# Performance work log

Hardware: AMD Instinct MI355X
Metric: run time of the kernel (lower is better)

Reference implementation:

```python
import jax, jax.numpy as jnp
import numpy as np

B = 8
FEAT = 256
HID = 256
NCLS = 80
SIZES = [(128, 128), (64, 64), (32, 32), (16, 16), (8, 8)]
DELTA_XY = 0.1   # dd_delta_range_xy
DELTA_WH = 2.0   # dd_delta_range_wh
PRIOR_P = 0.01   # prior_cls_prob


def _priors():
    # prior_cxcy: normalized grid centers per pyramid level (sine_pos_encodings id maps,
    # normalize=True with all-ones masks). prior_wh: (1/fW, 1/fH) per level.
    cxcy, wh = [], []
    for (h, w) in SIZES:
        cy = (jnp.arange(h, dtype=jnp.float32) + 0.5) / h
        cx = (jnp.arange(w, dtype=jnp.float32) + 0.5) / w
        gx, gy = jnp.meshgrid(cx, cy, indexing='xy')           # [h, w]
        cxcy.append(jnp.stack([gx, gy], axis=-1).reshape(h * w, 2))
        wh.append(jnp.broadcast_to(jnp.array([1.0 / w, 1.0 / h], jnp.float32), (h * w, 2)))
    return jnp.concatenate(cxcy, axis=0), jnp.concatenate(wh, axis=0)  # [N,2], [N,2]


def _mlp(x, Wh, bh, Wo, bo):
    # Linear(feat->hidden) + ReLU, then Linear(hidden->out)
    h = jax.nn.relu(jnp.einsum('bnf,hf->bnh', x, Wh) + bh)
    return jnp.einsum('bnh,oh->bno', h, Wo) + bo


def setup_inputs() -> dict:
    key = jax.random.key(0)
    ks = jax.random.split(key, 12)
    inp = {}
    for i, (h, w) in enumerate(SIZES):
        inp[f'fm{i}'] = jax.random.normal(ks[i], (B, FEAT, h, w), dtype=jnp.float32)
    s_in = 1.0 / np.sqrt(FEAT)
    s_h = 1.0 / np.sqrt(HID)
    bias_value = float(-np.log((1.0 - PRIOR_P) / PRIOR_P))
    inp['cls_Wh'] = jax.random.normal(ks[5], (HID, FEAT), dtype=jnp.float32) * s_in
    inp['cls_bh'] = jnp.zeros((HID,), jnp.float32)
    inp['cls_Wo'] = jax.random.normal(ks[6], (NCLS, HID), dtype=jnp.float32) * s_h
    inp['cls_bo'] = jnp.full((NCLS,), bias_value, jnp.float32)  # focal prior bias init
    inp['box_Wh'] = jax.random.normal(ks[7], (HID, FEAT), dtype=jnp.float32) * s_in
    inp['box_bh'] = jnp.zeros((HID,), jnp.float32)
    inp['box_Wo'] = jax.random.normal(ks[8], (4, HID), dtype=jnp.float32) * s_h
    inp['box_bo'] = jnp.zeros((4,), jnp.float32)  # zero-init box bias
    return inp


def reference(fm0, fm1, fm2, fm3, fm4,
              cls_Wh, cls_bh, cls_Wo, cls_bo,
              box_Wh, box_bh, box_Wo, box_bo):
    fms = [fm0, fm1, fm2, fm3, fm4]
    # obj_feats: concat of flatten(2).permute(0,2,1) -> [B, N, FEAT]
    obj_feats = jnp.concatenate(
        [f.reshape(B, FEAT, -1).transpose(0, 2, 1) for f in fms], axis=1)
    cls_logits = _mlp(obj_feats, cls_Wh, cls_bh, cls_Wo, cls_bo)   # [B, N, NCLS]
    box_logits = _mlp(obj_feats, box_Wh, box_bh, box_Wo, box_bo)   # [B, N, 4]
    box_deltas = jnp.tanh(box_logits)
    prior_cxcy, prior_wh = _priors()
    pred_cxcy = prior_cxcy[None] + DELTA_XY * box_deltas[:, :, :2]
    pred_wh = prior_wh[None] * (DELTA_WH ** box_deltas[:, :, 2:])
    # pack [cls_logits | pred_boxes(cxcywh)] -> [B, N, NCLS+4]
    return jnp.concatenate([cls_logits, pred_cxcy, pred_wh], axis=-1)
```

## Files before the change

kernel.cpp:

```cpp
#include <hip/hip_runtime.h>
#include <math.h>
#include <stdint.h>

#define NTOK 21824

typedef __attribute__((ext_vector_type(8)))  short bf16x8;
typedef __attribute__((ext_vector_type(4)))  float f32x4;
typedef __attribute__((ext_vector_type(16))) float f32x16;

__device__ __forceinline__ uint32_t f2bf(float f) {
    uint32_t u = __builtin_bit_cast(uint32_t, f);
    return (u + 0x7FFFu + ((u >> 16) & 1u)) >> 16;
}
__device__ __forceinline__ uint32_t pkbf(float lo, float hi) {
    return f2bf(lo) | (f2bf(hi) << 16);
}

#define WOFF_CWH 0
#define WOFF_BWH 65536
#define WOFF_CWO 131072
#define WOFF_BWO 151552

__global__ void prep_weights(const float* __restrict__ cWh, const float* __restrict__ cWo,
                             const float* __restrict__ bWh, const float* __restrict__ bWo,
                             uint16_t* __restrict__ ws) {
    int i = blockIdx.x * 256 + threadIdx.x;
    if (i >= 155648) return;
    uint32_t v;
    if (i < 65536)       v = f2bf(cWh[i]);
    else if (i < 131072) v = f2bf(bWh[i - 65536]);
    else if (i < 151552) v = f2bf(cWo[i - 131072]);
    else { int j = i - 151552; v = (j < 1024) ? f2bf(bWo[j]) : 0u; }
    ws[i] = (uint16_t)v;
}

__global__ __launch_bounds__(512, 4) void dfd_fused(
    const float* __restrict__ fm0, const float* __restrict__ fm1,
    const float* __restrict__ fm2, const float* __restrict__ fm3,
    const float* __restrict__ fm4,
    const float* __restrict__ cls_bh, const float* __restrict__ cls_bo,
    const float* __restrict__ box_bh, const float* __restrict__ box_bo,
    const uint16_t* __restrict__ wbf,
    float* __restrict__ out)
{
    __shared__ uint16_t LB[64 * 512];
    uint16_t* Xs = LB;
    uint16_t* Hs = LB;

    const int tid  = threadIdx.x;
    const int lane = tid & 63;
    const int w    = tid >> 6;
    const int r    = lane & 15;
    const int q    = lane >> 4;
    const int n0   = blockIdx.x * 64;
    const int b    = blockIdx.y;

    const float* fm; int off, ls;
    if      (n0 < 16384) { fm = fm0; off = 0;     ls = 7; }
    else if (n0 < 20480) { fm = fm1; off = 16384; ls = 6; }
    else if (n0 < 21504) { fm = fm2; off = 20480; ls = 5; }
    else if (n0 < 21760) { fm = fm3; off = 21504; ls = 4; }
    else                 { fm = fm4; off = 21760; ls = 3; }
    const int dim = 1 << ls;
    const int hw  = dim * dim;
    const int p0  = n0 - off;

    {
        const int t  = lane;
        const int sw = (t & 7) << 3;
        const float* src = fm + (size_t)b * 256 * hw + p0 + t;
        #pragma unroll
        for (int i = 0; i < 8; ++i) {
            const int f = w * 4 + i * 32;
            const float x0 = src[(size_t)(f + 0) * hw];
            const float x1 = src[(size_t)(f + 1) * hw];
            const float x2 = src[(size_t)(f + 2) * hw];
            const float x3 = src[(size_t)(f + 3) * hw];
            uint2 pk; pk.x = pkbf(x0, x1); pk.y = pkbf(x2, x3);
            *reinterpret_cast<uint2*>(&Xs[t * 256 + (f ^ sw)]) = pk;
        }
    }
    __syncthreads();

    f32x16 acc[2][2];
    {
        #pragma unroll
        for (int mt = 0; mt < 2; ++mt)
            #pragma unroll
            for (int h = 0; h < 2; ++h)
                #pragma unroll
                for (int e = 0; e < 16; ++e) acc[mt][h][e] = 0.f;

        const int col = lane & 31;
        const int kh  = (lane >> 5) * 8;
        const uint16_t* Wc = wbf + WOFF_CWH + (w * 32 + col) * 256 + kh;
        const uint16_t* Wb = wbf + WOFF_BWH + (w * 32 + col) * 256 + kh;

        #pragma unroll
        for (int ks = 0; ks < 16; ++ks) {
            const bf16x8 bc = *(const bf16x8*)(Wc + ks * 16);
            const bf16x8 bb = *(const bf16x8*)(Wb + ks * 16);
            #pragma unroll
            for (int mt = 0; mt < 2; ++mt) {
                const int t = mt * 32 + col;
                const int k = (ks * 16 + kh) ^ ((t & 7) << 3);
                const bf16x8 a = *(const bf16x8*)&Xs[t * 256 + k];
                acc[mt][0] = __builtin_amdgcn_mfma_f32_32x32x16_bf16(a, bc, acc[mt][0], 0, 0, 0);
                acc[mt][1] = __builtin_amdgcn_mfma_f32_32x32x16_bf16(a, bb, acc[mt][1], 0, 0, 0);
            }
        }
    }
    __syncthreads();

    {
        const int col  = lane & 31;
        const float bc = cls_bh[w * 32 + col];
        const float bbx = box_bh[w * 32 + col];
        #pragma unroll
        for (int mt = 0; mt < 2; ++mt) {
            #pragma unroll
            for (int reg = 0; reg < 16; ++reg) {
                const int t  = mt * 32 + (reg & 3) + 8 * (reg >> 2) + 4 * (lane >> 5);
                const int sw = (t & 7) << 3;
                const int hh = w * 32 + col;
                Hs[t * 512 + ((hh)       ^ sw)] = (uint16_t)f2bf(fmaxf(acc[mt][0][reg] + bc, 0.f));
                Hs[t * 512 + ((256 + hh) ^ sw)] = (uint16_t)f2bf(fmaxf(acc[mt][1][reg] + bbx, 0.f));
            }
        }
    }
    __syncthreads();

    if (w < 5) {
        f32x4 c[4];
        #pragma unroll
        for (int m = 0; m < 4; ++m) c[m] = {0.f, 0.f, 0.f, 0.f};
        const uint16_t* Bw = wbf + WOFF_CWO + (w * 16 + r) * 256 + q * 8;
        #pragma unroll
        for (int kq = 0; kq < 8; ++kq) {
            const bf16x8 bfr = *(const bf16x8*)(Bw + kq * 32);
            #pragma unroll
            for (int m = 0; m < 4; ++m) {
                const int t = m * 16 + r;
                const int kcol = (kq * 32 + q * 8) ^ ((t & 7) << 3);
                const bf16x8 a = *(const bf16x8*)&Hs[t * 512 + kcol];
                c[m] = __builtin_amdgcn_mfma_f32_16x16x32_bf16(a, bfr, c[m], 0, 0, 0);
            }
        }
        const float bo_l = cls_bo[w * 16 + r];
        #pragma unroll
        for (int m = 0; m < 4; ++m)
            #pragma unroll
            for (int jj = 0; jj < 4; ++jj)
                out[((size_t)b * NTOK + n0 + m * 16 + q * 4 + jj) * 84 + w * 16 + r]
                    = c[m][jj] + bo_l;
    } else if (w < 7) {
        const int m0 = (w - 5) * 2;
        f32x4 c[2];
        c[0] = {0.f, 0.f, 0.f, 0.f}; c[1] = {0.f, 0.f, 0.f, 0.f};
        const uint16_t* Bw = wbf + WOFF_BWO + r * 256 + q * 8;
        #pragma unroll
        for (int kq = 0; kq < 8; ++kq) {
            const bf16x8 bfr = *(const bf16x8*)(Bw + kq * 32);
            #pragma unroll
            for (int mm = 0; mm < 2; ++mm) {
                const int t = (m0 + mm) * 16 + r;
                const int kcol = 256 + ((kq * 32 + q * 8) ^ ((t & 7) << 3));
                const bf16x8 a = *(const bf16x8*)&Hs[t * 512 + kcol];
                c[mm] = __builtin_amdgcn_mfma_f32_16x16x32_bf16(a, bfr, c[mm], 0, 0, 0);
            }
        }
        if (r < 4) {
            const float bo_l = box_bo[r];
            const float inv  = 1.0f / (float)dim;
            #pragma unroll
            for (int mm = 0; mm < 2; ++mm)
                #pragma unroll
                for (int jj = 0; jj < 4; ++jj) {
                    const int t = (m0 + mm) * 16 + q * 4 + jj;
                    const int p = p0 + t;
                    const float d = tanhf(c[mm][jj] + bo_l);
                    float val;
                    if (r == 0)      val = ((float)(p & (dim - 1)) + 0.5f) * inv + 0.1f * d;
                    else if (r == 1) val = ((float)(p >> ls) + 0.5f) * inv + 0.1f * d;
                    else             val = exp2f(d) * inv;
                    out[((size_t)b * NTOK + n0 + t) * 84 + 80 + r] = val;
                }
        }
    }
}

extern "C" void kernel_launch(void* const* d_in, const int* in_sizes, int n_in,
                              void* d_out, int out_size, void* d_ws, size_t ws_size,
                              hipStream_t stream) {
    uint16_t* ws = (uint16_t*)d_ws;
    prep_weights<<<608, 256, 0, stream>>>(
        (const float*)d_in[5],  (const float*)d_in[7],
        (const float*)d_in[9],  (const float*)d_in[11], ws);
    dim3 grid(NTOK / 64, 8);
    dfd_fused<<<grid, 512, 0, stream>>>(
        (const float*)d_in[0], (const float*)d_in[1], (const float*)d_in[2],
        (const float*)d_in[3], (const float*)d_in[4],
        (const float*)d_in[6],  (const float*)d_in[8],
        (const float*)d_in[10], (const float*)d_in[12],
        ws, (float*)d_out);
}
```

Measured before the change: 136.3 us.

## Swap MFMA operand roles so outputs are row-contiguous and vectorize stores

Transposes both GEMM stages so weights are the A operand and tokens the B operand. Each lane then holds consecutive hidden units or classes for one token, which allows packed bf16x4 hidden writes to LDS and float4 global stores of the output rows. The second-stage work is rebalanced across all 8 waves, where before waves 7 were idle and waves 5-6 did the box head. It also switches to the HIP bf16 intrinsic for packing. The risk is extra weight-fragment loads per wave and divergent branches on mh.

```diff
diff --git a/kernel.cpp b/kernel.cpp
--- a/kernel.cpp
+++ b/kernel.cpp
@@ -1,4 +1,5 @@
 #include <hip/hip_runtime.h>
+#include <hip/hip_bf16.h>
 #include <math.h>
 #include <stdint.h>
 
@@ -12,8 +13,10 @@
     uint32_t u = __builtin_bit_cast(uint32_t, f);
     return (u + 0x7FFFu + ((u >> 16) & 1u)) >> 16;
 }
-__device__ __forceinline__ uint32_t pkbf(float lo, float hi) {
-    return f2bf(lo) | (f2bf(hi) << 16);
+__device__ __forceinline__ uint32_t pkbf2(float lo, float hi) {
+    __hip_bfloat162 h = __float22bfloat162_rn(float2{lo, hi});
+    uint32_t r; __builtin_memcpy(&r, &h, 4);
+    return r;
 }
 
 #define WOFF_CWH 0
@@ -52,6 +55,8 @@
     const int w    = tid >> 6;
     const int r    = lane & 15;
     const int q    = lane >> 4;
+    const int col  = lane & 31;
+    const int hi   = lane >> 5;
     const int n0   = blockIdx.x * 64;
     const int b    = blockIdx.y;
 
@@ -76,7 +81,7 @@
             const float x1 = src[(size_t)(f + 1) * hw];
             const float x2 = src[(size_t)(f + 2) * hw];
             const float x3 = src[(size_t)(f + 3) * hw];
-            uint2 pk; pk.x = pkbf(x0, x1); pk.y = pkbf(x2, x3);
+            uint2 pk; pk.x = pkbf2(x0, x1); pk.y = pkbf2(x2, x3);
             *reinterpret_cast<uint2*>(&Xs[t * 256 + (f ^ sw)]) = pk;
         }
     }
@@ -87,104 +92,114 @@
         #pragma unroll
         for (int mt = 0; mt < 2; ++mt)
             #pragma unroll
-            for (int h = 0; h < 2; ++h)
+            for (int nt = 0; nt < 2; ++nt)
                 #pragma unroll
-                for (int e = 0; e < 16; ++e) acc[mt][h][e] = 0.f;
-
-        const int col = lane & 31;
-        const int kh  = (lane >> 5) * 8;
-        const uint16_t* Wc = wbf + WOFF_CWH + (w * 32 + col) * 256 + kh;
-        const uint16_t* Wb = wbf + WOFF_BWH + (w * 32 + col) * 256 + kh;
+                for (int e = 0; e < 16; ++e) acc[mt][nt][e] = 0.f;
+
+        const int hh0 = w * 64;
+        const uint16_t* Wbase = (w < 4) ? wbf + WOFF_CWH + hh0 * 256
+                                        : wbf + WOFF_BWH + (hh0 - 256) * 256;
+        const int kh = hi * 8;
+        const uint16_t* Wr = Wbase + col * 256 + kh;
+        const int sw0 = (col & 7) << 3;
 
         #pragma unroll
         for (int ks = 0; ks < 16; ++ks) {
-            const bf16x8 bc = *(const bf16x8*)(Wc + ks * 16);
-            const bf16x8 bb = *(const bf16x8*)(Wb + ks * 16);
-            #pragma unroll
-            for (int mt = 0; mt < 2; ++mt) {
-                const int t = mt * 32 + col;
-                const int k = (ks * 16 + kh) ^ ((t & 7) << 3);
-                const bf16x8 a = *(const bf16x8*)&Xs[t * 256 + k];
-                acc[mt][0] = __builtin_amdgcn_mfma_f32_32x32x16_bf16(a, bc, acc[mt][0], 0, 0, 0);
-                acc[mt][1] = __builtin_amdgcn_mfma_f32_32x32x16_bf16(a, bb, acc[mt][1], 0, 0, 0);
-            }
+            const bf16x8 a0 = *(const bf16x8*)(Wr + ks * 16);
+            const bf16x8 a1 = *(const bf16x8*)(Wr + 8192 + ks * 16);
+            const int kx = (ks * 16 + kh) ^ sw0;
+            const bf16x8 x0 = *(const bf16x8*)&Xs[col * 256 + kx];
+            const bf16x8 x1 = *(const bf16x8*)&Xs[(32 + col) * 256 + kx];
+            acc[0][0] = __builtin_amdgcn_mfma_f32_32x32x16_bf16(a0, x0, acc[0][0], 0, 0, 0);
+            acc[0][1] = __builtin_amdgcn_mfma_f32_32x32x16_bf16(a0, x1, acc[0][1], 0, 0, 0);
+            acc[1][0] = __builtin_amdgcn_mfma_f32_32x32x16_bf16(a1, x0, acc[1][0], 0, 0, 0);
+            acc[1][1] = __builtin_amdgcn_mfma_f32_32x32x16_bf16(a1, x1, acc[1][1], 0, 0, 0);
         }
     }
     __syncthreads();
 
     {
-        const int col  = lane & 31;
-        const float bc = cls_bh[w * 32 + col];
-        const float bbx = box_bh[w * 32 + col];
+        const int hh0 = w * 64;
+        const float* bh_ = (w < 4) ? cls_bh + hh0 : box_bh + (hh0 - 256);
         #pragma unroll
         for (int mt = 0; mt < 2; ++mt) {
             #pragma unroll
-            for (int reg = 0; reg < 16; ++reg) {
-                const int t  = mt * 32 + (reg & 3) + 8 * (reg >> 2) + 4 * (lane >> 5);
-                const int sw = (t & 7) << 3;
-                const int hh = w * 32 + col;
-                Hs[t * 512 + ((hh)       ^ sw)] = (uint16_t)f2bf(fmaxf(acc[mt][0][reg] + bc, 0.f));
-                Hs[t * 512 + ((256 + hh) ^ sw)] = (uint16_t)f2bf(fmaxf(acc[mt][1][reg] + bbx, 0.f));
+            for (int nt = 0; nt < 2; ++nt) {
+                const int t   = nt * 32 + col;
+                const int swt = (t & 7) << 3;
+                #pragma unroll
+                for (int g = 0; g < 4; ++g) {
+                    const int hb = mt * 32 + 8 * g + 4 * hi;
+                    const f32x4 bv = *(const f32x4*)(bh_ + hb);
+                    const float v0 = fmaxf(acc[mt][nt][4 * g + 0] + bv[0], 0.f);
+                    const float v1 = fmaxf(acc[mt][nt][4 * g + 1] + bv[1], 0.f);
+                    const float v2 = fmaxf(acc[mt][nt][4 * g + 2] + bv[2], 0.f);
+                    const float v3 = fmaxf(acc[mt][nt][4 * g + 3] + bv[3], 0.f);
+                    uint2 pk; pk.x = pkbf2(v0, v1); pk.y = pkbf2(v2, v3);
+                    *reinterpret_cast<uint2*>(&Hs[t * 512 + ((hh0 + hb) ^ swt)]) = pk;
+                }
             }
         }
     }
     __syncthreads();
 
-    if (w < 5) {
-        f32x4 c[4];
-        #pragma unroll
-        for (int m = 0; m < 4; ++m) c[m] = {0.f, 0.f, 0.f, 0.f};
-        const uint16_t* Bw = wbf + WOFF_CWO + (w * 16 + r) * 256 + q * 8;
+    {
+        const int nt2 = w & 3;
+        const int mh  = w >> 2;
+        const int t   = nt2 * 16 + r;
+        const int swt = (t & 7) << 3;
+        const uint16_t* hrow = &Hs[t * 512];
+
+        f32x4 c[3];
+        c[0] = {0.f,0.f,0.f,0.f}; c[1] = {0.f,0.f,0.f,0.f}; c[2] = {0.f,0.f,0.f,0.f};
+        const int m0 = mh * 3;
+        const uint16_t* WoA = wbf + WOFF_CWO + r * 256 + q * 8;
+        const uint16_t* WoB = wbf + WOFF_BWO + r * 256 + q * 8;
+
         #pragma unroll
         for (int kq = 0; kq < 8; ++kq) {
-            const bf16x8 bfr = *(const bf16x8*)(Bw + kq * 32);
-            #pragma unroll
-            for (int m = 0; m < 4; ++m) {
-                const int t = m * 16 + r;
-                const int kcol = (kq * 32 + q * 8) ^ ((t & 7) << 3);
-                const bf16x8 a = *(const bf16x8*)&Hs[t * 512 + kcol];
-                c[m] = __builtin_amdgcn_mfma_f32_16x16x32_bf16(a, bfr, c[m], 0, 0, 0);
+            const bf16x8 hb = *(const bf16x8*)&hrow[(kq * 32 + q * 8) ^ swt];
+            const bf16x8 aA = *(const bf16x8*)(WoA + (m0 + 0) * 4096 + kq * 32);
+            const bf16x8 aB = *(const bf16x8*)(WoA + (m0 + 1) * 4096 + kq * 32);
+            c[0] = __builtin_amdgcn_mfma_f32_16x16x32_bf16(aA, hb, c[0], 0, 0, 0);
+            c[1] = __builtin_amdgcn_mfma_f32_16x16x32_bf16(aB, hb, c[1], 0, 0, 0);
+            if (mh == 0) {
+                const bf16x8 aC = *(const bf16x8*)(WoA + 2 * 4096 + kq * 32);
+                c[2] = __builtin_amdgcn_mfma_f32_16x16x32_bf16(aC, hb, c[2], 0, 0, 0);
+            } else {
+                const bf16x8 hbb = *(const bf16x8*)&hrow[(256 + kq * 32 + q * 8) ^ swt];
+                const bf16x8 aC  = *(const bf16x8*)(WoB + kq * 32);
+                c[2] = __builtin_amdgcn_mfma_f32_16x16x32_bf16(aC, hbb, c[2], 0, 0, 0);
             }
         }
-        const float bo_l = cls_bo[w * 16 + r];
-        #pragma unroll
-        for (int m = 0; m < 4; ++m)
-            #pragma unroll
-            for (int jj = 0; jj < 4; ++jj)
-                out[((size_t)b * NTOK + n0 + m * 16 + q * 4 + jj) * 84 + w * 16 + r]
-                    = c[m][jj] + bo_l;
-    } else if (w < 7) {
-        const int m0 = (w - 5) * 2;
-        f32x4 c[2];
-        c[0] = {0.f, 0.f, 0.f, 0.f}; c[1] = {0.f, 0.f, 0.f, 0.f};
-        const uint16_t* Bw = wbf + WOFF_BWO + r * 256 + q * 8;
-        #pragma unroll
-        for (int kq = 0; kq < 8; ++kq) {
-            const bf16x8 bfr = *(const bf16x8*)(Bw + kq * 32);
-            #pragma unroll
-            for (int mm = 0; mm < 2; ++mm) {
-                const int t = (m0 + mm) * 16 + r;
-                const int kcol = 256 + ((kq * 32 + q * 8) ^ ((t & 7) << 3));
-                const bf16x8 a = *(const bf16x8*)&Hs[t * 512 + kcol];
-                c[mm] = __builtin_amdgcn_mfma_f32_16x16x32_bf16(a, bfr, c[mm], 0, 0, 0);
+
+        float* orow = out + ((size_t)b * NTOK + n0 + t) * 84;
+        const int ncls = (mh == 0) ? 3 : 2;
+        #pragma unroll
+        for (int i = 0; i < 3; ++i) {
+            if (i < ncls) {
+                const int m = m0 + i;
+                const f32x4 bo = *(const f32x4*)(cls_bo + m * 16 + q * 4);
+                f32x4 v;
+                #pragma unroll
+                for (int jj = 0; jj < 4; ++jj) v[jj] = c[i][jj] + bo[jj];
+                *(f32x4*)(orow + m * 16 + q * 4) = v;
             }
         }
-        if (r < 4) {
-            const float bo_l = box_bo[r];
-            const float inv  = 1.0f / (float)dim;
-            #pragma unroll
-            for (int mm = 0; mm < 2; ++mm)
-                #pragma unroll
-                for (int jj = 0; jj < 4; ++jj) {
-                    const int t = (m0 + mm) * 16 + q * 4 + jj;
-                    const int p = p0 + t;
-                    const float d = tanhf(c[mm][jj] + bo_l);
-                    float val;
-                    if (r == 0)      val = ((float)(p & (dim - 1)) + 0.5f) * inv + 0.1f * d;
-                    else if (r == 1) val = ((float)(p >> ls) + 0.5f) * inv + 0.1f * d;
-                    else             val = exp2f(d) * inv;
-                    out[((size_t)b * NTOK + n0 + t) * 84 + 80 + r] = val;
-                }
+        if (mh == 1 && q == 0) {
+            const f32x4 bo = *(const f32x4*)box_bo;
+            const float inv = 1.0f / (float)dim;
+            const int p = p0 + t;
+            const float d0 = tanhf(c[2][0] + bo[0]);
+            const float d1 = tanhf(c[2][1] + bo[1]);
+            const float d2 = tanhf(c[2][2] + bo[2]);
+            const float d3 = tanhf(c[2][3] + bo[3]);
+            f32x4 v;
+            v[0] = ((float)(p & (dim - 1)) + 0.5f) * inv + 0.1f * d0;
+            v[1] = ((float)(p >> ls) + 0.5f) * inv + 0.1f * d1;
+            v[2] = exp2f(d2) * inv;
+            v[3] = exp2f(d3) * inv;
+            *(f32x4*)(orow + 80) = v;
         }
     }
 }
```

After: 182.0 us. 1.34x slower.

## Make blocks persistent over four token tiles and prefetch next tile's features into registers

Applied to the files above, without the earlier changes.

Each block now handles four consecutive 64-token tiles instead of one, shrinking the grid to 86x8. The next tile's fp32 feature loads are issued into registers before the current tile's MFMA work, so global latency overlaps compute. The bf16 packing of inputs also switches to the hip_bf16 paired conversion intrinsic. The cost is 32 extra live registers per thread and fewer blocks (688) to spread over the CUs, which may hurt occupancy and load balance.

```diff
diff --git a/kernel.cpp b/kernel.cpp
--- a/kernel.cpp
+++ b/kernel.cpp
@@ -1,8 +1,12 @@
 #include <hip/hip_runtime.h>
+#include <hip/hip_bf16.h>
 #include <math.h>
 #include <stdint.h>
 
 #define NTOK 21824
+#define NTILES 341
+#define NITER 4
+#define GRIDX 86
 
 typedef __attribute__((ext_vector_type(8)))  short bf16x8;
 typedef __attribute__((ext_vector_type(4)))  float f32x4;
@@ -12,8 +16,10 @@
     uint32_t u = __builtin_bit_cast(uint32_t, f);
     return (u + 0x7FFFu + ((u >> 16) & 1u)) >> 16;
 }
-__device__ __forceinline__ uint32_t pkbf(float lo, float hi) {
-    return f2bf(lo) | (f2bf(hi) << 16);
+__device__ __forceinline__ uint32_t pkbf2(float lo, float hi) {
+    __hip_bfloat162 h = __float22bfloat162_rn(float2{lo, hi});
+    uint32_t r; __builtin_memcpy(&r, &h, 4);
+    return r;
 }
 
 #define WOFF_CWH 0
@@ -52,140 +58,171 @@
     const int w    = tid >> 6;
     const int r    = lane & 15;
     const int q    = lane >> 4;
-    const int n0   = blockIdx.x * 64;
+    const int col  = lane & 31;
+    const int hi   = lane >> 5;
     const int b    = blockIdx.y;
 
-    const float* fm; int off, ls;
-    if      (n0 < 16384) { fm = fm0; off = 0;     ls = 7; }
-    else if (n0 < 20480) { fm = fm1; off = 16384; ls = 6; }
-    else if (n0 < 21504) { fm = fm2; off = 20480; ls = 5; }
-    else if (n0 < 21760) { fm = fm3; off = 21504; ls = 4; }
-    else                 { fm = fm4; off = 21760; ls = 3; }
-    const int dim = 1 << ls;
-    const int hw  = dim * dim;
-    const int p0  = n0 - off;
-
-    {
-        const int t  = lane;
-        const int sw = (t & 7) << 3;
-        const float* src = fm + (size_t)b * 256 * hw + p0 + t;
+    auto lookup = [&](int n0, const float*& fm, int& off, int& ls) {
+        if      (n0 < 16384) { fm = fm0; off = 0;     ls = 7; }
+        else if (n0 < 20480) { fm = fm1; off = 16384; ls = 6; }
+        else if (n0 < 21504) { fm = fm2; off = 20480; ls = 5; }
+        else if (n0 < 21760) { fm = fm3; off = 21504; ls = 4; }
+        else                 { fm = fm4; off = 21760; ls = 3; }
+    };
+
+    float xr[32];
+    auto load_x = [&](int tl) {
+        const float* fmp; int offp, lsp;
+        const int nn = tl * 64;
+        lookup(nn, fmp, offp, lsp);
+        const int hwp = 1 << (2 * lsp);
+        const float* src = fmp + (size_t)b * 256 * hwp + (nn - offp) + lane;
         #pragma unroll
         for (int i = 0; i < 8; ++i) {
             const int f = w * 4 + i * 32;
-            const float x0 = src[(size_t)(f + 0) * hw];
-            const float x1 = src[(size_t)(f + 1) * hw];
-            const float x2 = src[(size_t)(f + 2) * hw];
-            const float x3 = src[(size_t)(f + 3) * hw];
-            uint2 pk; pk.x = pkbf(x0, x1); pk.y = pkbf(x2, x3);
-            *reinterpret_cast<uint2*>(&Xs[t * 256 + (f ^ sw)]) = pk;
-        }
-    }
-    __syncthreads();
-
-    f32x16 acc[2][2];
-    {
-        #pragma unroll
-        for (int mt = 0; mt < 2; ++mt)
-            #pragma unroll
-            for (int h = 0; h < 2; ++h)
-                #pragma unroll
-                for (int e = 0; e < 16; ++e) acc[mt][h][e] = 0.f;
-
-        const int col = lane & 31;
-        const int kh  = (lane >> 5) * 8;
-        const uint16_t* Wc = wbf + WOFF_CWH + (w * 32 + col) * 256 + kh;
-        const uint16_t* Wb = wbf + WOFF_BWH + (w * 32 + col) * 256 + kh;
-
-        #pragma unroll
-        for (int ks = 0; ks < 16; ++ks) {
-            const bf16x8 bc = *(const bf16x8*)(Wc + ks * 16);
-            const bf16x8 bb = *(const bf16x8*)(Wb + ks * 16);
+            #pragma unroll
+            for (int e = 0; e < 4; ++e)
+                xr[i * 4 + e] = src[(size_t)(f + e) * hwp];
+        }
+    };
+
+    const int base = blockIdx.x * NITER;
+    load_x(base < NTILES ? base : NTILES - 1);
+
+    for (int it = 0; it < NITER; ++it) {
+        const int tile = base + it;
+        if (tile >= NTILES) break;
+        const int n0 = tile * 64;
+        const float* fmc; int off, ls;
+        lookup(n0, fmc, off, ls);
+        const int dim = 1 << ls;
+        const int p0  = n0 - off;
+
+        {
+            const int t  = lane;
+            const int sw = (t & 7) << 3;
+            #pragma unroll
+            for (int i = 0; i < 8; ++i) {
+                const int f = w * 4 + i * 32;
+                uint2 pk;
+                pk.x = pkbf2(xr[i * 4 + 0], xr[i * 4 + 1]);
+                pk.y = pkbf2(xr[i * 4 + 2], xr[i * 4 + 3]);
+                *reinterpret_cast<uint2*>(&Xs[t * 256 + (f ^ sw)]) = pk;
+            }
+        }
+        __syncthreads();
+
+        if (it + 1 < NITER) {
+            int nt_ = tile + 1;
+            if (nt_ > NTILES - 1) nt_ = NTILES - 1;
+            load_x(nt_);
+        }
+
+        f32x16 acc[2][2];
+        {
+            #pragma unroll
+            for (int mt = 0; mt < 2; ++mt)
+                #pragma unroll
+                for (int h = 0; h < 2; ++h)
+                    #pragma unroll
+                    for (int e = 0; e < 16; ++e) acc[mt][h][e] = 0.f;
+
+            const int rowoff = (w * 32 + col) * 256;
+            const int kh = hi * 8;
+            const uint16_t* Wc = wbf + WOFF_CWH + rowoff + kh;
+            const uint16_t* Wb = wbf + WOFF_BWH + rowoff + kh;
+            const int sw0 = (col & 7) << 3;
+
+            #pragma unroll
+            for (int ks = 0; ks < 16; ++ks) {
+                const bf16x8 bc = *(const bf16x8*)(Wc + ks * 16);
+                const bf16x8 bb = *(const bf16x8*)(Wb + ks * 16);
+                const int kx = (ks * 16 + kh) ^ sw0;
+                const bf16x8 x0 = *(const bf16x8*)&Xs[col * 256 + kx];
+                const bf16x8 x1 = *(const bf16x8*)&Xs[(32 + col) * 256 + kx];
+                acc[0][0] = __builtin_amdgcn_mfma_f32_32x32x16_bf16(x0, bc, acc[0][0], 0, 0, 0);
+                acc[0][1] = __builtin_amdgcn_mfma_f32_32x32x16_bf16(x0, bb, acc[0][1], 0, 0, 0);
+                acc[1][0] = __builtin_amdgcn_mfma_f32_32x32x16_bf16(x1, bc, acc[1][0], 0, 0, 0);
+                acc[1][1] = __builtin_amdgcn_mfma_f32_32x32x16_bf16(x1, bb, acc[1][1], 0, 0, 0);
+            }
+        }
+        __syncthreads();
+
+        {
+            const float bc  = cls_bh[w * 32 + col];
+            const float bbx = box_bh[w * 32 + col];
+            const int hh = w * 32 + col;
             #pragma unroll
             for (int mt = 0; mt < 2; ++mt) {
-                const int t = mt * 32 + col;
-                const int k = (ks * 16 + kh) ^ ((t & 7) << 3);
-                const bf16x8 a = *(const bf16x8*)&Xs[t * 256 + k];
-                acc[mt][0] = __builtin_amdgcn_mfma_f32_32x32x16_bf16(a, bc, acc[mt][0], 0, 0, 0);
-                acc[mt][1] = __builtin_amdgcn_mfma_f32_32x32x16_bf16(a, bb, acc[mt][1], 0, 0, 0);
-            }
-        }
-    }
-    __syncthreads();
-
-    {
-        const int col  = lane & 31;
-        const float bc = cls_bh[w * 32 + col];
-        const float bbx = box_bh[w * 32 + col];
-        #pragma unroll
-        for (int mt = 0; mt < 2; ++mt) {
-            #pragma unroll
-            for (int reg = 0; reg < 16; ++reg) {
-                const int t  = mt * 32 + (reg & 3) + 8 * (reg >> 2) + 4 * (lane >> 5);
-                const int sw = (t & 7) << 3;
-                const int hh = w * 32 + col;
-                Hs[t * 512 + ((hh)       ^ sw)] = (uint16_t)f2bf(fmaxf(acc[mt][0][reg] + bc, 0.f));
-                Hs[t * 512 + ((256 + hh) ^ sw)] = (uint16_t)f2bf(fmaxf(acc[mt][1][reg] + bbx, 0.f));
-            }
-        }
-    }
-    __syncthreads();
-
-    if (w < 5) {
-        f32x4 c[4];
-        #pragma unroll
-        for (int m = 0; m < 4; ++m) c[m] = {0.f, 0.f, 0.f, 0.f};
-        const uint16_t* Bw = wbf + WOFF_CWO + (w * 16 + r) * 256 + q * 8;
-        #pragma unroll
-        for (int kq = 0; kq < 8; ++kq) {
-            const bf16x8 bfr = *(const bf16x8*)(Bw + kq * 32);
-            #pragma unroll
-            for (int m = 0; m < 4; ++m) {
-                const int t = m * 16 + r;
-                const int kcol = (kq * 32 + q * 8) ^ ((t & 7) << 3);
-                const bf16x8 a = *(const bf16x8*)&Hs[t * 512 + kcol];
-                c[m] = __builtin_amdgcn_mfma_f32_16x16x32_bf16(a, bfr, c[m], 0, 0, 0);
-            }
-        }
-        const float bo_l = cls_bo[w * 16 + r];
-        #pragma unroll
-        for (int m = 0; m < 4; ++m)
-            #pragma unroll
-            for (int jj = 0; jj < 4; ++jj)
-                out[((size_t)b * NTOK + n0 + m * 16 + q * 4 + jj) * 84 + w * 16 + r]
-                    = c[m][jj] + bo_l;
-    } else if (w < 7) {
-        const int m0 = (w - 5) * 2;
-        f32x4 c[2];
-        c[0] = {0.f, 0.f, 0.f, 0.f}; c[1] = {0.f, 0.f, 0.f, 0.f};
-        const uint16_t* Bw = wbf + WOFF_BWO + r * 256 + q * 8;
-        #pragma unroll
-        for (int kq = 0; kq < 8; ++kq) {
-            const bf16x8 bfr = *(const bf16x8*)(Bw + kq * 32);
-            #pragma unroll
-            for (int mm = 0; mm < 2; ++mm) {
-                const int t = (m0 + mm) * 16 + r;
-                const int kcol = 256 + ((kq * 32 + q * 8) ^ ((t & 7) << 3));
-                const bf16x8 a = *(const bf16x8*)&Hs[t * 512 + kcol];
-                c[mm] = __builtin_amdgcn_mfma_f32_16x16x32_bf16(a, bfr, c[mm], 0, 0, 0);
-            }
-        }
-        if (r < 4) {
-            const float bo_l = box_bo[r];
-            const float inv  = 1.0f / (float)dim;
-            #pragma unroll
-            for (int mm = 0; mm < 2; ++mm)
-                #pragma unroll
-                for (int jj = 0; jj < 4; ++jj) {
-                    const int t = (m0 + mm) * 16 + q * 4 + jj;
-                    const int p = p0 + t;
-                    const float d = tanhf(c[mm][jj] + bo_l);
-                    float val;
-                    if (r == 0)      val = ((float)(p & (dim - 1)) + 0.5f) * inv + 0.1f * d;
-                    else if (r == 1) val = ((float)(p >> ls) + 0.5f) * inv + 0.1f * d;
-                    else             val = exp2f(d) * inv;
-                    out[((size_t)b * NTOK + n0 + t) * 84 + 80 + r] = val;
+                #pragma unroll
+                for (int reg = 0; reg < 16; ++reg) {
+                    const int t  = mt * 32 + (reg & 3) + 8 * (reg >> 2) + 4 * hi;
+                    const int sw = (t & 7) << 3;
+                    Hs[t * 512 + ((hh)       ^ sw)] = (uint16_t)f2bf(fmaxf(acc[mt][0][reg] + bc,  0.f));
+                    Hs[t * 512 + ((256 + hh) ^ sw)] = (uint16_t)f2bf(fmaxf(acc[mt][1][reg] + bbx, 0.f));
                 }
-        }
+            }
+        }
+        __syncthreads();
+
+        if (w < 5) {
+            f32x4 c[4];
+            #pragma unroll
+            for (int m = 0; m < 4; ++m) c[m] = {0.f, 0.f, 0.f, 0.f};
+            const uint16_t* Bw = wbf + WOFF_CWO + (w * 16 + r) * 256 + q * 8;
+            #pragma unroll
+            for (int kq = 0; kq < 8; ++kq) {
+                const bf16x8 bfr = *(const bf16x8*)(Bw + kq * 32);
+                #pragma unroll
+                for (int m = 0; m < 4; ++m) {
+                    const int t = m * 16 + r;
+                    const int kcol = (kq * 32 + q * 8) ^ ((t & 7) << 3);
+                    const bf16x8 a = *(const bf16x8*)&Hs[t * 512 + kcol];
+                    c[m] = __builtin_amdgcn_mfma_f32_16x16x32_bf16(a, bfr, c[m], 0, 0, 0);
+                }
+            }
+            const float bo_l = cls_bo[w * 16 + r];
+            #pragma unroll
+            for (int m = 0; m < 4; ++m)
+                #pragma unroll
+                for (int jj = 0; jj < 4; ++jj)
+                    out[((size_t)b * NTOK + n0 + m * 16 + q * 4 + jj) * 84 + w * 16 + r]
+                        = c[m][jj] + bo_l;
+        } else if (w < 7) {
+            const int m0 = (w - 5) * 2;
+            f32x4 c[2];
+            c[0] = {0.f, 0.f, 0.f, 0.f}; c[1] = {0.f, 0.f, 0.f, 0.f};
+            const uint16_t* Bw = wbf + WOFF_BWO + r * 256 + q * 8;
+            #pragma unroll
+            for (int kq = 0; kq < 8; ++kq) {
+                const bf16x8 bfr = *(const bf16x8*)(Bw + kq * 32);
+                #pragma unroll
+                for (int mm = 0; mm < 2; ++mm) {
+                    const int t = (m0 + mm) * 16 + r;
+                    const int kcol = 256 + ((kq * 32 + q * 8) ^ ((t & 7) << 3));
+                    const bf16x8 a = *(const bf16x8*)&Hs[t * 512 + kcol];
+                    c[mm] = __builtin_amdgcn_mfma_f32_16x16x32_bf16(a, bfr, c[mm], 0, 0, 0);
+                }
+            }
+            if (r < 4) {
+                const float bo_l = box_bo[r];
+                const float inv  = 1.0f / (float)dim;
+                #pragma unroll
+                for (int mm = 0; mm < 2; ++mm)
+                    #pragma unroll
+                    for (int jj = 0; jj < 4; ++jj) {
+                        const int t = (m0 + mm) * 16 + q * 4 + jj;
+                        const int p = p0 + t;
+                        const float d = tanhf(c[mm][jj] + bo_l);
+                        float val;
+                        if (r == 0)      val = ((float)(p & (dim - 1)) + 0.5f) * inv + 0.1f * d;
+                        else if (r == 1) val = ((float)(p >> ls) + 0.5f) * inv + 0.1f * d;
+                        else             val = exp2f(d) * inv;
+                        out[((size_t)b * NTOK + n0 + t) * 84 + 80 + r] = val;
+                    }
+            }
+        }
+        __syncthreads();
     }
 }
 
@@ -196,7 +233,7 @@
     prep_weights<<<608, 256, 0, stream>>>(
         (const float*)d_in[5],  (const float*)d_in[7],
         (const float*)d_in[9],  (const float*)d_in[11], ws);
-    dim3 grid(NTOK / 64, 8);
+    dim3 grid(GRIDX, 8);
     dfd_fused<<<grid, 512, 0, stream>>>(
         (const float*)d_in[0], (const float*)d_in[1], (const float*)d_in[2],
         (const float*)d_in[3], (const float*)d_in[4],
```

Result: slower. 521.9 us (+282.9%).

## Transpose first-layer MFMA operands so hidden outputs pack into vectorized LDS stores

Applied to the files above, without the earlier changes.

The first GEMM swaps operand roles: weights become the A operand (64 hidden units per wave, with cls waves 0-3 and box waves 4-7) and tokens become B. Each lane then holds four consecutive hidden values per token, so the bias+ReLU epilogue loads biases as float4 and writes packed 8-byte bf16 stores to LDS instead of scalar 16-bit stores. The input staging also loads 8 features per thread and writes 16-byte LDS stores, and it uses the HIP bf16x2 conversion intrinsic. This is meant to cut LDS store instruction count and conversion overhead. It changes the weight fetch pattern to two 32-row blocks per wave.

```diff
diff --git a/kernel.cpp b/kernel.cpp
--- a/kernel.cpp
+++ b/kernel.cpp
@@ -1,4 +1,5 @@
 #include <hip/hip_runtime.h>
+#include <hip/hip_bf16.h>
 #include <math.h>
 #include <stdint.h>
 
@@ -12,8 +13,10 @@
     uint32_t u = __builtin_bit_cast(uint32_t, f);
     return (u + 0x7FFFu + ((u >> 16) & 1u)) >> 16;
 }
-__device__ __forceinline__ uint32_t pkbf(float lo, float hi) {
-    return f2bf(lo) | (f2bf(hi) << 16);
+__device__ __forceinline__ uint32_t pkbf2(float lo, float hi) {
+    __hip_bfloat162 h = __float22bfloat162_rn(float2{lo, hi});
+    uint32_t r; __builtin_memcpy(&r, &h, 4);
+    return r;
 }
 
 #define WOFF_CWH 0
@@ -52,6 +55,8 @@
     const int w    = tid >> 6;
     const int r    = lane & 15;
     const int q    = lane >> 4;
+    const int col  = lane & 31;
+    const int hi   = lane >> 5;
     const int n0   = blockIdx.x * 64;
     const int b    = blockIdx.y;
 
@@ -70,14 +75,15 @@
         const int sw = (t & 7) << 3;
         const float* src = fm + (size_t)b * 256 * hw + p0 + t;
         #pragma unroll
-        for (int i = 0; i < 8; ++i) {
-            const int f = w * 4 + i * 32;
-            const float x0 = src[(size_t)(f + 0) * hw];
-            const float x1 = src[(size_t)(f + 1) * hw];
-            const float x2 = src[(size_t)(f + 2) * hw];
-            const float x3 = src[(size_t)(f + 3) * hw];
-            uint2 pk; pk.x = pkbf(x0, x1); pk.y = pkbf(x2, x3);
-            *reinterpret_cast<uint2*>(&Xs[t * 256 + (f ^ sw)]) = pk;
+        for (int i = 0; i < 4; ++i) {
+            const int f0 = w * 8 + i * 64;
+            float x[8];
+            #pragma unroll
+            for (int e = 0; e < 8; ++e) x[e] = src[(size_t)(f0 + e) * hw];
+            uint4 pk;
+            pk.x = pkbf2(x[0], x[1]); pk.y = pkbf2(x[2], x[3]);
+            pk.z = pkbf2(x[4], x[5]); pk.w = pkbf2(x[6], x[7]);
+            *reinterpret_cast<uint4*>(&Xs[t * 256 + (f0 ^ sw)]) = pk;
         }
     }
     __syncthreads();
@@ -87,44 +93,52 @@
         #pragma unroll
         for (int mt = 0; mt < 2; ++mt)
             #pragma unroll
-            for (int h = 0; h < 2; ++h)
+            for (int nt = 0; nt < 2; ++nt)
                 #pragma unroll
-                for (int e = 0; e < 16; ++e) acc[mt][h][e] = 0.f;
-
-        const int col = lane & 31;
-        const int kh  = (lane >> 5) * 8;
-        const uint16_t* Wc = wbf + WOFF_CWH + (w * 32 + col) * 256 + kh;
-        const uint16_t* Wb = wbf + WOFF_BWH + (w * 32 + col) * 256 + kh;
+                for (int e = 0; e < 16; ++e) acc[mt][nt][e] = 0.f;
+
+        const int hh0 = w * 64;
+        const uint16_t* Wbase = (w < 4) ? wbf + WOFF_CWH + hh0 * 256
+                                        : wbf + WOFF_BWH + (hh0 - 256) * 256;
+        const int kh = hi * 8;
+        const uint16_t* Wr = Wbase + col * 256 + kh;
+        const int sw0 = (col & 7) << 3;
 
         #pragma unroll
         for (int ks = 0; ks < 16; ++ks) {
-            const bf16x8 bc = *(const bf16x8*)(Wc + ks * 16);
-            const bf16x8 bb = *(const bf16x8*)(Wb + ks * 16);
-            #pragma unroll
-            for (int mt = 0; mt < 2; ++mt) {
-                const int t = mt * 32 + col;
-                const int k = (ks * 16 + kh) ^ ((t & 7) << 3);
-                const bf16x8 a = *(const bf16x8*)&Xs[t * 256 + k];
-                acc[mt][0] = __builtin_amdgcn_mfma_f32_32x32x16_bf16(a, bc, acc[mt][0], 0, 0, 0);
-                acc[mt][1] = __builtin_amdgcn_mfma_f32_32x32x16_bf16(a, bb, acc[mt][1], 0, 0, 0);
-            }
+            const bf16x8 a0 = *(const bf16x8*)(Wr + ks * 16);
+            const bf16x8 a1 = *(const bf16x8*)(Wr + 8192 + ks * 16);
+            const int kx = (ks * 16 + kh) ^ sw0;
+            const bf16x8 x0 = *(const bf16x8*)&Xs[col * 256 + kx];
+            const bf16x8 x1 = *(const bf16x8*)&Xs[(32 + col) * 256 + kx];
+            acc[0][0] = __builtin_amdgcn_mfma_f32_32x32x16_bf16(a0, x0, acc[0][0], 0, 0, 0);
+            acc[0][1] = __builtin_amdgcn_mfma_f32_32x32x16_bf16(a0, x1, acc[0][1], 0, 0, 0);
+            acc[1][0] = __builtin_amdgcn_mfma_f32_32x32x16_bf16(a1, x0, acc[1][0], 0, 0, 0);
+            acc[1][1] = __builtin_amdgcn_mfma_f32_32x32x16_bf16(a1, x1, acc[1][1], 0, 0, 0);
         }
     }
     __syncthreads();
 
     {
-        const int col  = lane & 31;
-        const float bc = cls_bh[w * 32 + col];
-        const float bbx = box_bh[w * 32 + col];
+        const int hh0 = w * 64;
+        const float* bh_ = (w < 4) ? cls_bh + hh0 : box_bh + (hh0 - 256);
         #pragma unroll
         for (int mt = 0; mt < 2; ++mt) {
             #pragma unroll
-            for (int reg = 0; reg < 16; ++reg) {
-                const int t  = mt * 32 + (reg & 3) + 8 * (reg >> 2) + 4 * (lane >> 5);
-                const int sw = (t & 7) << 3;
-                const int hh = w * 32 + col;
-                Hs[t * 512 + ((hh)       ^ sw)] = (uint16_t)f2bf(fmaxf(acc[mt][0][reg] + bc, 0.f));
-                Hs[t * 512 + ((256 + hh) ^ sw)] = (uint16_t)f2bf(fmaxf(acc[mt][1][reg] + bbx, 0.f));
+            for (int nt = 0; nt < 2; ++nt) {
+                const int t   = nt * 32 + col;
+                const int swt = (t & 7) << 3;
+                #pragma unroll
+                for (int g = 0; g < 4; ++g) {
+                    const int hb = mt * 32 + 8 * g + 4 * hi;
+                    const f32x4 bv = *(const f32x4*)(bh_ + hb);
+                    const float v0 = fmaxf(acc[mt][nt][4 * g + 0] + bv[0], 0.f);
+                    const float v1 = fmaxf(acc[mt][nt][4 * g + 1] + bv[1], 0.f);
+                    const float v2 = fmaxf(acc[mt][nt][4 * g + 2] + bv[2], 0.f);
+                    const float v3 = fmaxf(acc[mt][nt][4 * g + 3] + bv[3], 0.f);
+                    uint2 pk; pk.x = pkbf2(v0, v1); pk.y = pkbf2(v2, v3);
+                    *reinterpret_cast<uint2*>(&Hs[t * 512 + ((hh0 + hb) ^ swt)]) = pk;
+                }
             }
         }
     }
```

Result: no change. 135.7 us (-0.5%).
